# Kernel tuning notes

Hardware: AMD Instinct MI355X
Metric: run time of the kernel (lower is better)

## Reference

```python
import jax, jax.numpy as jnp
import numpy as np

N_PITCH, N_DUR, N_TIME, N_VEL = 128, 160, 100, 128
VOCAB = N_PITCH + N_DUR + N_TIME + N_VEL  # 516
B, S = 32, 2048


def _build_vocab_tables():
    # token_type: 0='p', 1='d', 2='t', 3='v'; token_value: numeric suffix of itos_vocab[i]
    tt = np.concatenate([
        np.full(N_PITCH, 0), np.full(N_DUR, 1), np.full(N_TIME, 2), np.full(N_VEL, 3)
    ]).astype(np.int32)
    tv = np.concatenate([
        np.arange(N_PITCH), np.arange(N_DUR), np.arange(N_TIME), np.arange(N_VEL)
    ]).astype(np.float32)
    return jnp.asarray(tt), jnp.asarray(tv)


def setup_inputs() -> dict:
    key = jax.random.key(0)
    k1, k2, k3, k4 = jax.random.split(key, 4)
    token_type, token_value = _build_vocab_tables()
    return {
        "output": jax.random.normal(k1, (B, VOCAB, S), dtype=jnp.float32),
        "target": jax.random.randint(k2, (B, S), 0, VOCAB, dtype=jnp.int32),
        "token_type": token_type,
        "token_value": token_value,
        "coeff": jnp.asarray([0.5, 0.6, 0.2, 0.2], dtype=jnp.float32),
        "harmonic": jnp.asarray([0.6, 0.6, 0.2, 0.2, 0.2, 0.2, 1.5], dtype=jnp.float32),
    }


def _penalty_mask(pred, target, token_type, token_value, coeff, harmonic):
    pt, tt = token_type[pred], token_type[target]      # [B,S] type codes
    pv, tv = token_value[pred], token_value[target]    # [B,S] numeric values
    d = jnp.abs(pv - tv)
    # pitch: harmonic-interval weights (values are integer-valued floats -> exact ==)
    pitch_w = jnp.where(d == 7, harmonic[0],
              jnp.where(d == 5, harmonic[1],
              jnp.where(d == 3, harmonic[2],
              jnp.where(d == 4, harmonic[3],
              jnp.where(d == 1, harmonic[4],
              jnp.where(d == 2, harmonic[5], harmonic[6]))))))
    dur_w = coeff[1] * d / 160.0
    time_w = coeff[2] * d / 100.0
    vel_w = coeff[3] * d / 128.0
    same_type_w = jnp.where(pt == 0, pitch_w,
                  jnp.where(pt == 1, dur_w,
                  jnp.where(pt == 2, time_w, vel_w)))
    return jnp.where(pt != tt, coeff[0], same_type_w)


def reference(output, target, token_type, token_value, coeff, harmonic):
    # Faithful to original: softmax over last (seq) axis, then argmax over vocab axis 1
    sm = jax.nn.softmax(output, axis=-1)
    pred = jnp.argmax(sm, axis=1)                      # [B,S]
    # mean cross-entropy over B*S (class axis = 1)
    logp = jax.nn.log_softmax(output, axis=1)          # [B,V,S]
    nll = -jnp.take_along_axis(logp, target[:, None, :], axis=1)[:, 0, :]
    loss = nll.mean()
    mask = _penalty_mask(pred, target, token_type, token_value, coeff, harmonic)
    high_cost = (loss * mask).mean()
    return loss + high_cost
```

## Files before the change

### kernel.cpp

```cpp
#include <hip/hip_runtime.h>

#define BB 32
#define SS 2048
#define VV 516
#define NBS (BB * SS)
#define NCHUNK 16
#define NPART 256

__device__ inline float waveReduceSum(float v) {
    #pragma unroll
    for (int o = 32; o > 0; o >>= 1) v += __shfl_down(v, o, 64);
    return v;
}

__global__ __launch_bounds__(512, 4) void hl_tile(const float* __restrict__ x,
                                                  const int* __restrict__ target,
                                                  int* __restrict__ ctr,
                                                  float* __restrict__ pSum,
                                                  float* __restrict__ pBest,
                                                  int* __restrict__ pIdx,
                                                  float* __restrict__ xtArr) {
    __shared__ float ldsE[8 * 2048];
    __shared__ float sRcp[8];

    if (blockIdx.x == 0 && threadIdx.x == 0) ctr[0] = 0;

    const int c = blockIdx.x & 15, b = blockIdx.x >> 4;
    const int v0 = 32 * c + (c > 12 ? c - 12 : 0);
    const int nv = (c >= 12) ? 33 : 32;
    const int tid = threadIdx.x, lane = tid & 63, wv = tid >> 6;

    const int s0 = tid << 2;
    const int bs = b * SS + s0;
    int4 tg4 = *(const int4*)(target + bs);
    int tg[4] = {tg4.x, tg4.y, tg4.z, tg4.w};

    float sum[4], best[4], xt[4];
    int bi[4];
    #pragma unroll
    for (int i = 0; i < 4; ++i) { sum[i] = 0.f; best[i] = -1.f; bi[i] = v0; xt[i] = 0.f; }

    const float* xb = x + (size_t)(b * VV + v0) * SS;

    for (int vs = 0; vs < nv; vs += 8) {
        int m = nv - vs; if (m > 8) m = 8;
        if (wv < m) {
            const float* row = xb + (size_t)(vs + wv) * SS;
            float4 v[8];
            #pragma unroll
            for (int j = 0; j < 8; ++j)
                v[j] = *(const float4*)(row + j * 256 + lane * 4);
            float a0 = 0.f, a1 = 0.f, a2 = 0.f, a3 = 0.f;
            #pragma unroll
            for (int j = 0; j < 8; ++j) {
                float4 e;
                e.x = __expf(v[j].x); e.y = __expf(v[j].y);
                e.z = __expf(v[j].z); e.w = __expf(v[j].w);
                *(float4*)(ldsE + wv * 2048 + j * 256 + lane * 4) = e;
                a0 += e.x; a1 += e.y; a2 += e.z; a3 += e.w;
            }
            float ssum = waveReduceSum((a0 + a1) + (a2 + a3));
            if (lane == 0) sRcp[wv] = 1.f / ssum;
        }
        __syncthreads();
        for (int v = 0; v < m; ++v) {
            float r = sRcp[v];
            int vg = v0 + vs + v;
            float4 e4 = *(const float4*)(ldsE + v * 2048 + s0);
            float e[4] = {e4.x, e4.y, e4.z, e4.w};
            #pragma unroll
            for (int i = 0; i < 4; ++i) {
                sum[i] += e[i];
                float sc = e[i] * r;
                if (sc > best[i]) { best[i] = sc; bi[i] = vg; }
            }
        }
        #pragma unroll
        for (int i = 0; i < 4; ++i) {
            int lr = tg[i] - (v0 + vs);
            if (lr >= 0 && lr < m) xt[i] = __logf(ldsE[lr * 2048 + s0 + i]);
        }
        __syncthreads();
    }

    int o = c * NBS + bs;
    *(float4*)(pSum + o)  = make_float4(sum[0], sum[1], sum[2], sum[3]);
    *(float4*)(pBest + o) = make_float4(best[0], best[1], best[2], best[3]);
    *(int4*)(pIdx + o)    = make_int4(bi[0], bi[1], bi[2], bi[3]);
    int v1 = v0 + nv;
    #pragma unroll
    for (int i = 0; i < 4; ++i)
        if (tg[i] >= v0 && tg[i] < v1) xtArr[bs + i] = xt[i];
}

__global__ __launch_bounds__(256) void hl_comb(const int* __restrict__ target,
                                               const int* __restrict__ ttype,
                                               const float* __restrict__ tval,
                                               const float* __restrict__ coeff,
                                               const float* __restrict__ harm,
                                               const float* __restrict__ pSum,
                                               const float* __restrict__ pBest,
                                               const int* __restrict__ pIdx,
                                               const float* __restrict__ xtArr,
                                               float* __restrict__ pNll,
                                               float* __restrict__ pMask,
                                               int* __restrict__ counter,
                                               float* __restrict__ outv) {
    __shared__ float lds[8];
    __shared__ bool isLast;
    int idx = blockIdx.x * 256 + threadIdx.x;

    float sum = 0.f, best = -1e30f;
    int bestIdx = 0;
    #pragma unroll
    for (int c = 0; c < NCHUNK; ++c) {
        int o = c * NBS + idx;
        sum += pSum[o];
        float sc = pBest[o];
        int ii = pIdx[o];
        if (sc > best) { best = sc; bestIdx = ii; }
    }
    int tgt = target[idx];
    float nll = __logf(sum) - xtArr[idx];

    int pt = ttype[bestIdx], tt = ttype[tgt];
    float pv = tval[bestIdx], tv = tval[tgt];
    float d = fabsf(pv - tv);
    float pw = (d == 7.f) ? harm[0] : (d == 5.f) ? harm[1] : (d == 3.f) ? harm[2]
             : (d == 4.f) ? harm[3] : (d == 1.f) ? harm[4] : (d == 2.f) ? harm[5]
             : harm[6];
    float w = (pt == 0) ? pw
            : (pt == 1) ? coeff[1] * d * (1.f / 160.f)
            : (pt == 2) ? coeff[2] * d * (1.f / 100.f)
            :             coeff[3] * d * (1.f / 128.f);
    float mask = (pt != tt) ? coeff[0] : w;

    int lane = threadIdx.x & 63, wvv = threadIdx.x >> 6;
    float rn = waveReduceSum(nll);
    if (lane == 0) lds[wvv] = rn;
    __syncthreads();
    float totN = (threadIdx.x == 0) ? lds[0] + lds[1] + lds[2] + lds[3] : 0.f;
    __syncthreads();
    float rm = waveReduceSum(mask);
    if (lane == 0) lds[wvv] = rm;
    __syncthreads();
    if (threadIdx.x == 0) {
        pNll[blockIdx.x]  = totN;
        pMask[blockIdx.x] = lds[0] + lds[1] + lds[2] + lds[3];
        __threadfence();
        unsigned old = atomicAdd((unsigned*)counter, 1u);
        isLast = (old == NPART - 1);
    }
    __syncthreads();
    if (isLast) {
        __threadfence();
        int t = threadIdx.x;
        float n = waveReduceSum(pNll[t]);
        float m = waveReduceSum(pMask[t]);
        if (lane == 0) { lds[wvv] = n; lds[4 + wvv] = m; }
        __syncthreads();
        if (t == 0) {
            float tn = lds[0] + lds[1] + lds[2] + lds[3];
            float tm = lds[4] + lds[5] + lds[6] + lds[7];
            const float inv = 1.f / (float)NBS;
            outv[0] = (tn * inv) * (1.f + tm * inv);
        }
    }
}

extern "C" void kernel_launch(void* const* d_in, const int* in_sizes, int n_in,
                              void* d_out, int out_size, void* d_ws, size_t ws_size,
                              hipStream_t stream) {
    const float* x      = (const float*)d_in[0];
    const int*   target = (const int*)d_in[1];
    const int*   ttype  = (const int*)d_in[2];
    const float* tval   = (const float*)d_in[3];
    const float* coeff  = (const float*)d_in[4];
    const float* harm   = (const float*)d_in[5];

    float* ws    = (float*)d_ws;
    int*   ctr   = (int*)ws;
    float* pNll  = ws + 4;
    float* pMask = pNll + NPART;
    float* xtArr = pMask + NPART;
    float* pSum  = xtArr + NBS;
    float* pBest = pSum + (size_t)NCHUNK * NBS;
    int*   pIdx  = (int*)(pBest + (size_t)NCHUNK * NBS);

    hl_tile<<<BB * NCHUNK, 512, 0, stream>>>(x, target, ctr, pSum, pBest,
                                             pIdx, xtArr);
    hl_comb<<<NBS / 256, 256, 0, stream>>>(target, ttype, tval, coeff, harm,
                                           pSum, pBest, pIdx, xtArr,
                                           pNll, pMask, ctr, (float*)d_out);
}
```

Baseline: 46.98 us.

## Double-buffer vocab rows via direct global-to-LDS async loads in tile kernel

Replaces register-staged row loads with global_load_lds into a double-buffered LDS tile of 4 rows, prefetching the next 4 rows while computing exp, row sums and argmax on the current ones. Each row is now split across two waves, and the 33rd row for the last chunks is handled in a separate tail path read straight from global memory. Launch bounds change from 4 to 2 blocks per SM. The goal is to overlap HBM latency with compute, at the cost of lower occupancy and hand-placed waitcnt and barriers.

```diff
diff --git a/kernel.cpp b/kernel.cpp
--- a/kernel.cpp
+++ b/kernel.cpp
@@ -7,21 +7,29 @@
 #define NCHUNK 16
 #define NPART 256
 
-__device__ inline float waveReduceSum(float v) {
+__device__ __forceinline__ float waveReduceSum(float v) {
     #pragma unroll
     for (int o = 32; o > 0; o >>= 1) v += __shfl_down(v, o, 64);
     return v;
 }
 
-__global__ __launch_bounds__(512, 4) void hl_tile(const float* __restrict__ x,
+__device__ __forceinline__ void stage16(const float* g, float* l) {
+    __builtin_amdgcn_global_load_lds(
+        (const __attribute__((address_space(1))) void*)(g),
+        (__attribute__((address_space(3))) void*)(l),
+        16, 0, 0);
+}
+
+__global__ __launch_bounds__(512, 2) void hl_tile(const float* __restrict__ x,
                                                   const int* __restrict__ target,
                                                   int* __restrict__ ctr,
                                                   float* __restrict__ pSum,
                                                   float* __restrict__ pBest,
                                                   int* __restrict__ pIdx,
                                                   float* __restrict__ xtArr) {
-    __shared__ float ldsE[8 * 2048];
-    __shared__ float sRcp[8];
+    __shared__ float buf[2][4][2048];
+    __shared__ float ldsH[2][4][2];
+    __shared__ float ldsT[8];
 
     if (blockIdx.x == 0 && threadIdx.x == 0) ctr[0] = 0;
 
@@ -29,58 +37,102 @@
     const int v0 = 32 * c + (c > 12 ? c - 12 : 0);
     const int nv = (c >= 12) ? 33 : 32;
     const int tid = threadIdx.x, lane = tid & 63, wv = tid >> 6;
-
+    const int row = wv >> 1, half = wv & 1;
     const int s0 = tid << 2;
     const int bs = b * SS + s0;
+
     int4 tg4 = *(const int4*)(target + bs);
     int tg[4] = {tg4.x, tg4.y, tg4.z, tg4.w};
 
-    float sum[4], best[4], xt[4];
-    int bi[4];
-    #pragma unroll
-    for (int i = 0; i < 4; ++i) { sum[i] = 0.f; best[i] = -1.f; bi[i] = v0; xt[i] = 0.f; }
-
-    const float* xb = x + (size_t)(b * VV + v0) * SS;
-
-    for (int vs = 0; vs < nv; vs += 8) {
-        int m = nv - vs; if (m > 8) m = 8;
-        if (wv < m) {
-            const float* row = xb + (size_t)(vs + wv) * SS;
-            float4 v[8];
+    float sum[4]  = {0.f, 0.f, 0.f, 0.f};
+    float best[4] = {-1.f, -1.f, -1.f, -1.f};
+    float xt[4]   = {0.f, 0.f, 0.f, 0.f};
+    int   bi[4]   = {v0, v0, v0, v0};
+
+    const float* gbase = x + (size_t)(b * VV + v0 + row) * SS + half * 1024 + lane * 4;
+
+    {
+        float* ls = &buf[0][row][half * 1024];
+        #pragma unroll
+        for (int j = 0; j < 4; ++j) stage16(gbase + j * 256, ls + j * 256);
+    }
+    asm volatile("s_waitcnt vmcnt(0)" ::: "memory");
+    __builtin_amdgcn_sched_barrier(0);
+    __builtin_amdgcn_s_barrier();
+
+    for (int k = 0; k < 8; ++k) {
+        const int kb = k & 1;
+        if (k + 1 < 8) {
+            const float* gs = gbase + (size_t)(k + 1) * 4 * SS;
+            float* ls = &buf[kb ^ 1][row][half * 1024];
             #pragma unroll
-            for (int j = 0; j < 8; ++j)
-                v[j] = *(const float4*)(row + j * 256 + lane * 4);
-            float a0 = 0.f, a1 = 0.f, a2 = 0.f, a3 = 0.f;
+            for (int j = 0; j < 4; ++j) stage16(gs + j * 256, ls + j * 256);
+        }
+        {
+            float* p = &buf[kb][row][half * 1024 + lane * 4];
+            float a = 0.f;
             #pragma unroll
-            for (int j = 0; j < 8; ++j) {
+            for (int j = 0; j < 4; ++j) {
+                float4 v = *(const float4*)(p + j * 256);
                 float4 e;
-                e.x = __expf(v[j].x); e.y = __expf(v[j].y);
-                e.z = __expf(v[j].z); e.w = __expf(v[j].w);
-                *(float4*)(ldsE + wv * 2048 + j * 256 + lane * 4) = e;
-                a0 += e.x; a1 += e.y; a2 += e.z; a3 += e.w;
+                e.x = __expf(v.x); e.y = __expf(v.y);
+                e.z = __expf(v.z); e.w = __expf(v.w);
+                *(float4*)(p + j * 256) = e;
+                a += (e.x + e.y) + (e.z + e.w);
             }
-            float ssum = waveReduceSum((a0 + a1) + (a2 + a3));
-            if (lane == 0) sRcp[wv] = 1.f / ssum;
-        }
-        __syncthreads();
-        for (int v = 0; v < m; ++v) {
-            float r = sRcp[v];
-            int vg = v0 + vs + v;
-            float4 e4 = *(const float4*)(ldsE + v * 2048 + s0);
-            float e[4] = {e4.x, e4.y, e4.z, e4.w};
-            #pragma unroll
-            for (int i = 0; i < 4; ++i) {
-                sum[i] += e[i];
-                float sc = e[i] * r;
-                if (sc > best[i]) { best[i] = sc; bi[i] = vg; }
-            }
+            a = waveReduceSum(a);
+            if (lane == 0) ldsH[kb][row][half] = a;
+        }
+        asm volatile("s_waitcnt lgkmcnt(0)" ::: "memory");
+        __builtin_amdgcn_sched_barrier(0);
+        __builtin_amdgcn_s_barrier();
+        #pragma unroll
+        for (int r = 0; r < 4; ++r) {
+            float rs = ldsH[kb][r][0] + ldsH[kb][r][1];
+            float rc = 1.f / rs;
+            int vg = v0 + k * 4 + r;
+            float4 e = *(const float4*)&buf[kb][r][s0];
+            sum[0] += e.x; sum[1] += e.y; sum[2] += e.z; sum[3] += e.w;
+            float c0 = e.x * rc, c1 = e.y * rc, c2 = e.z * rc, c3 = e.w * rc;
+            if (c0 > best[0]) { best[0] = c0; bi[0] = vg; }
+            if (c1 > best[1]) { best[1] = c1; bi[1] = vg; }
+            if (c2 > best[2]) { best[2] = c2; bi[2] = vg; }
+            if (c3 > best[3]) { best[3] = c3; bi[3] = vg; }
         }
         #pragma unroll
         for (int i = 0; i < 4; ++i) {
-            int lr = tg[i] - (v0 + vs);
-            if (lr >= 0 && lr < m) xt[i] = __logf(ldsE[lr * 2048 + s0 + i]);
-        }
-        __syncthreads();
+            int lr = tg[i] - (v0 + k * 4);
+            if (lr >= 0 && lr < 4) xt[i] = __logf(buf[kb][lr][s0 + i]);
+        }
+        asm volatile("s_waitcnt vmcnt(0)" ::: "memory");
+        __builtin_amdgcn_sched_barrier(0);
+        __builtin_amdgcn_s_barrier();
+    }
+
+    if (nv == 33) {
+        int vg = v0 + 32;
+        float4 xv = *(const float4*)(x + (size_t)(b * VV + vg) * SS + s0);
+        float4 e;
+        e.x = __expf(xv.x); e.y = __expf(xv.y);
+        e.z = __expf(xv.z); e.w = __expf(xv.w);
+        float a = waveReduceSum((e.x + e.y) + (e.z + e.w));
+        if (lane == 0) ldsT[wv] = a;
+        asm volatile("s_waitcnt lgkmcnt(0)" ::: "memory");
+        __builtin_amdgcn_sched_barrier(0);
+        __builtin_amdgcn_s_barrier();
+        float rs = ((ldsT[0] + ldsT[1]) + (ldsT[2] + ldsT[3]))
+                 + ((ldsT[4] + ldsT[5]) + (ldsT[6] + ldsT[7]));
+        float rc = 1.f / rs;
+        if (vg == tg[0]) xt[0] = xv.x;
+        if (vg == tg[1]) xt[1] = xv.y;
+        if (vg == tg[2]) xt[2] = xv.z;
+        if (vg == tg[3]) xt[3] = xv.w;
+        sum[0] += e.x; sum[1] += e.y; sum[2] += e.z; sum[3] += e.w;
+        float c0 = e.x * rc, c1 = e.y * rc, c2 = e.z * rc, c3 = e.w * rc;
+        if (c0 > best[0]) { best[0] = c0; bi[0] = vg; }
+        if (c1 > best[1]) { best[1] = c1; bi[1] = vg; }
+        if (c2 > best[2]) { best[2] = c2; bi[2] = vg; }
+        if (c3 > best[3]) { best[3] = c3; bi[3] = vg; }
     }
 
     int o = c * NBS + bs;
```

Result: no change. 47.27 us (+0.6%).
